# Kernel optimization log

Measured on AMD Instinct MI355X. Metric: run time of the kernel, lower is better.

Reference implementation:

```python
import jax, jax.numpy as jnp
import numpy as np

B, N, IN_DIM, OUT_DIM, MID_DIM, K = 4, 8192, 3, 64, 32, 16
EPS = 1e-5  # BatchNorm eps


def _bn_relu(x, gamma, beta):
    # x: [B, N, C]; BatchNorm1d in training mode -> batch stats over (B, N)
    mean = jnp.mean(x, axis=(0, 1))
    var = jnp.var(x, axis=(0, 1))
    return jax.nn.relu(gamma * (x - mean) * jax.lax.rsqrt(var + EPS) + beta)


def _gather(pts, idx):
    # pts: [B, N, C]; idx: [B, ...] int -> [B, ..., C]
    return jax.vmap(lambda p, i: p[i])(pts, idx)


def _fps(xyz, npoint):
    # farthest point sampling; xyz: [B, N, 3] -> idx [B, npoint]
    b, n, _ = xyz.shape

    def step(carry, _):
        dist, farthest = carry
        centroid = jnp.take_along_axis(xyz, farthest[:, None, None], axis=1)  # [B,1,3]
        d = jnp.sum((xyz - centroid) ** 2, axis=-1)  # [B,N]
        dist = jnp.minimum(dist, d)
        nxt = jnp.argmax(dist, axis=-1).astype(jnp.int32)
        return (dist, nxt), farthest

    init = (jnp.full((b, n), 1e10, xyz.dtype), jnp.zeros((b,), jnp.int32))
    _, idx = jax.lax.scan(step, init, None, length=npoint)
    return idx.T  # [B, npoint]


def _knn(query, ref, k):
    # query: [B,S,3], ref: [B,N,3] -> k nearest indices [B,S,k]
    d = (jnp.sum(query ** 2, -1, keepdims=True)
         - 2.0 * jnp.einsum('bsd,bnd->bsn', query, ref)
         + jnp.sum(ref ** 2, -1)[:, None, :])
    _, idx = jax.lax.top_k(-d, k)
    return idx


def setup_inputs() -> dict:
    key = jax.random.key(0)
    ks = jax.random.split(key, 13)
    sc = lambda fan_in: 1.0 / np.sqrt(fan_in)
    inp = {
        'x_in': jax.random.normal(ks[0], (B, N, IN_DIM), jnp.float32),
        # first_mlp: Conv1d(3,32,1) -> BN -> ReLU -> Conv1d(32,64,1)
        'W1': jax.random.uniform(ks[1], (MID_DIM, IN_DIM), jnp.float32, -sc(IN_DIM), sc(IN_DIM)),
        'b1': jax.random.uniform(ks[2], (MID_DIM,), jnp.float32, -sc(IN_DIM), sc(IN_DIM)),
        'g1': jnp.ones((MID_DIM,), jnp.float32),
        'be1': jnp.zeros((MID_DIM,), jnp.float32),
        'W2': jax.random.uniform(ks[3], (OUT_DIM, MID_DIM), jnp.float32, -sc(MID_DIM), sc(MID_DIM)),
        'b2': jax.random.uniform(ks[4], (OUT_DIM,), jnp.float32, -sc(MID_DIM), sc(MID_DIM)),
        # last_mlp: Conv1d(67,64,1) -> BN -> ReLU -> Conv1d(64,64,1)
        'W3': jax.random.uniform(ks[5], (OUT_DIM, OUT_DIM + IN_DIM), jnp.float32, -sc(OUT_DIM + IN_DIM), sc(OUT_DIM + IN_DIM)),
        'b3': jax.random.uniform(ks[6], (OUT_DIM,), jnp.float32, -sc(OUT_DIM + IN_DIM), sc(OUT_DIM + IN_DIM)),
        'g2': jnp.ones((OUT_DIM,), jnp.float32),
        'be2': jnp.zeros((OUT_DIM,), jnp.float32),
        'W4': jax.random.uniform(ks[7], (OUT_DIM, OUT_DIM), jnp.float32, -sc(OUT_DIM), sc(OUT_DIM)),
        'b4': jax.random.uniform(ks[8], (OUT_DIM,), jnp.float32, -sc(OUT_DIM), sc(OUT_DIM)),
    }
    return inp


def reference(x_in, W1, b1, g1, be1, W2, b2, W3, b3, g2, be2, W4, b4):
    # first_mlp (1x1 convs == per-point matmuls), [B,N,3] -> [B,N,64]
    h = _bn_relu(x_in @ W1.T + b1, g1, be1)
    feat = h @ W2.T + b2  # [B,N,64]

    # sample_and_group: FPS to N//2 centers, kNN grouping (indices are non-diff)
    xyz_c = jax.lax.stop_gradient(x_in)
    npoint = N // 2
    fidx = _fps(xyz_c, npoint)                      # [B,S]
    new_xyz = _gather(x_in, fidx)                   # [B,S,3]
    idx = _knn(_gather(xyz_c, fidx), xyz_c, K)      # [B,S,K]

    grouped_xyz = _gather(x_in, idx) - new_xyz[:, :, None, :]  # [B,S,K,3]
    grouped_feat = _gather(feat, idx)                          # [B,S,K,64]
    x_cat = jnp.concatenate([grouped_xyz, grouped_feat], axis=-1)  # [B,S,K,67]

    x = jnp.max(x_cat, axis=2)  # max over neighbors -> [B,S,67]

    # last_mlp, [B,S,67] -> [B,S,64]
    x = _bn_relu(x @ W3.T + b3, g2, be2)
    return x @ W4.T + b4
```

## Files before the change

### kernel.cpp

```cpp
#include <hip/hip_runtime.h>
#include <float.h>
#include <math.h>

#define NB 4
#define NPTS 8192
#define NS 4096
#define MIDC 32
#define OUTC 64
#define CATC 67
#define BN_EPS 1e-5f
#define TOTAL_PTS (NB*NPTS)
#define TOTAL_S (NB*NS)


__device__ __forceinline__ double packkey(double d, int sp) {
    return __longlong_as_double((__double_as_longlong(d) & 0xFFFFFFFFFFFFE000ULL)
                                | (unsigned long long)sp);
}

template<int CTRL, int RM>
__device__ __forceinline__ double dpp_fmax64(double v) {
    int lo = __builtin_amdgcn_update_dpp(0, __double2loint(v), CTRL, RM, 0xF, false);
    int hi = __builtin_amdgcn_update_dpp(0, __double2hiint(v), CTRL, RM, 0xF, false);
    return fmax(v, __hiloint2double(hi, lo));
}

__global__ void k_first(const float* __restrict__ xin, const float* __restrict__ W1,
                        const float* __restrict__ b1, float* __restrict__ t1) {
    int p = blockIdx.x * blockDim.x + threadIdx.x;
    float x = xin[p * 3], y = xin[p * 3 + 1], z = xin[p * 3 + 2];
#pragma unroll
    for (int c = 0; c < MIDC; c++) {
        float v = fmaf(W1[c * 3 + 2], z, fmaf(W1[c * 3 + 1], y, fmaf(W1[c * 3], x, b1[c])));
        t1[c * TOTAL_PTS + p] = v;
    }
}

__global__ void k_stats1(const float* __restrict__ t1, float* __restrict__ stats) {
    int c = blockIdx.x, tid = threadIdx.x;
    if (tid < 8) stats[64 + c * 8 + tid] = 0.f;
    float s = 0.f, ss = 0.f;
    for (int i = tid; i < TOTAL_PTS; i += 256) {
        float v = t1[c * TOTAL_PTS + i];
        s += v; ss = fmaf(v, v, ss);
    }
#pragma unroll
    for (int off = 32; off; off >>= 1) { s += __shfl_down(s, off); ss += __shfl_down(ss, off); }
    __shared__ float ls[4], lss[4];
    int w = tid >> 6, lane = tid & 63;
    if (lane == 0) { ls[w] = s; lss[w] = ss; }
    __syncthreads();
    if (tid == 0) {
        s = ls[0] + ls[1] + ls[2] + ls[3];
        ss = lss[0] + lss[1] + lss[2] + lss[3];
        float m = s / (float)TOTAL_PTS;
        float var = ss / (float)TOTAL_PTS - m * m;
        stats[c] = m;
        stats[32 + c] = rsqrtf(var + BN_EPS);
    }
}

__global__ void __launch_bounds__(256) k_feat(const float* __restrict__ t1, const float* __restrict__ stats,
                                              const float* __restrict__ g1, const float* __restrict__ be1,
                                              const float* __restrict__ W2, const float* __restrict__ b2,
                                              float* __restrict__ feat) {
    __shared__ float W2s[OUTC * MIDC];
    for (int i = threadIdx.x; i < OUTC * MIDC; i += 256) W2s[i] = W2[i];
    __syncthreads();
    int p = blockIdx.x * blockDim.x + threadIdx.x;
    float h[MIDC];
#pragma unroll
    for (int c = 0; c < MIDC; c++) {
        float v = t1[c * TOTAL_PTS + p];
        v = fmaf((v - stats[c]) * stats[32 + c], g1[c], be1[c]);
        h[c] = fmaxf(v, 0.f);
    }
#pragma unroll 4
    for (int o = 0; o < OUTC; o++) {
        float a = b2[o];
#pragma unroll
        for (int c = 0; c < MIDC; c++) a = fmaf(W2s[o * MIDC + c], h[c], a);
        feat[p * OUTC + o] = a;
    }
}

__device__ __forceinline__ unsigned int mpart(unsigned int x) {
    x &= 1023u;
    x = (x | (x << 16)) & 0x030000FFu;
    x = (x | (x << 8))  & 0x0300F00Fu;
    x = (x | (x << 4))  & 0x030C30C3u;
    x = (x | (x << 2))  & 0x09249249u;
    return x;
}

__global__ void __launch_bounds__(1024, 4) k_fps(const float* __restrict__ xin, int* __restrict__ fidx) {
    const int b = blockIdx.x;
    const int tid = threadIdx.x;
    const int lane = tid & 63, w = tid >> 6;
    const float* xb = xin + (size_t)b * NPTS * 3;
    __shared__ union UU {
        struct SS {
            float4 spts[NPTS];
            double swd[2][16];
            float  bbx[16][6];
        } s;
        unsigned long long karr[NPTS];
    } u;

    float mnx = FLT_MAX, mny = FLT_MAX, mnz = FLT_MAX;
    float mxx = -FLT_MAX, mxy = -FLT_MAX, mxz = -FLT_MAX;
    for (int j = 0; j < 8; j++) {
        int p = tid + (j << 10);
        float x = xb[p * 3], y = xb[p * 3 + 1], z = xb[p * 3 + 2];
        mnx = fminf(mnx, x); mny = fminf(mny, y); mnz = fminf(mnz, z);
        mxx = fmaxf(mxx, x); mxy = fmaxf(mxy, y); mxz = fmaxf(mxz, z);
    }
#pragma unroll
    for (int off = 32; off; off >>= 1) {
        mnx = fminf(mnx, __shfl_xor(mnx, off)); mny = fminf(mny, __shfl_xor(mny, off));
        mnz = fminf(mnz, __shfl_xor(mnz, off));
        mxx = fmaxf(mxx, __shfl_xor(mxx, off)); mxy = fmaxf(mxy, __shfl_xor(mxy, off));
        mxz = fmaxf(mxz, __shfl_xor(mxz, off));
    }
    if (lane == 0) {
        u.s.bbx[w][0] = mnx; u.s.bbx[w][1] = mny; u.s.bbx[w][2] = mnz;
        u.s.bbx[w][3] = mxx; u.s.bbx[w][4] = mxy; u.s.bbx[w][5] = mxz;
    }
    __syncthreads();
#pragma unroll
    for (int i = 0; i < 16; i++) {
        mnx = fminf(mnx, u.s.bbx[i][0]); mny = fminf(mny, u.s.bbx[i][1]);
        mnz = fminf(mnz, u.s.bbx[i][2]);
        mxx = fmaxf(mxx, u.s.bbx[i][3]); mxy = fmaxf(mxy, u.s.bbx[i][4]);
        mxz = fmaxf(mxz, u.s.bbx[i][5]);
    }
    float scx = 1023.0f / fmaxf(mxx - mnx, 1e-20f);
    float scy = 1023.0f / fmaxf(mxy - mny, 1e-20f);
    float scz = 1023.0f / fmaxf(mxz - mnz, 1e-20f);
    __syncthreads();

    for (int j = 0; j < 8; j++) {
        int p = tid + (j << 10);
        float x = xb[p * 3], y = xb[p * 3 + 1], z = xb[p * 3 + 2];
        unsigned int ix = (unsigned int)min(1023, max(0, (int)((x - mnx) * scx)));
        unsigned int iy = (unsigned int)min(1023, max(0, (int)((y - mny) * scy)));
        unsigned int iz = (unsigned int)min(1023, max(0, (int)((z - mnz) * scz)));
        unsigned long long code = (unsigned long long)((mpart(ix) << 2) | (mpart(iy) << 1) | mpart(iz));
        u.karr[p] = (code << 13) | (unsigned long long)p;
    }
    __syncthreads();
    for (int k = 2; k <= NPTS; k <<= 1) {
        for (int jj = k >> 1; jj > 0; jj >>= 1) {
            for (int pos = tid; pos < NPTS; pos += 1024) {
                int l2 = pos ^ jj;
                if (l2 > pos) {
                    unsigned long long a = u.karr[pos], c = u.karr[l2];
                    bool up = ((pos & k) == 0);
                    if ((up && a > c) || (!up && a < c)) { u.karr[pos] = c; u.karr[l2] = a; }
                }
            }
            __syncthreads();
        }
    }

    unsigned long long kk[8];
#pragma unroll
    for (int j = 0; j < 8; j++) kk[j] = u.karr[tid * 8 + j];
    __syncthreads();
    float blox = FLT_MAX, bloy = FLT_MAX, bloz = FLT_MAX;
    float bhix = -FLT_MAX, bhiy = -FLT_MAX, bhiz = -FLT_MAX;
    float prx[8], pry[8], prz[8];
    double dk[8];
#pragma unroll
    for (int j = 0; j < 8; j++) {
        int oi = (int)(kk[j] & 0x1FFFULL);
        float x = xb[oi * 3], y = xb[oi * 3 + 1], z = xb[oi * 3 + 2];
        int sp = tid * 8 + j;
        int slot = (sp >> 3) | ((sp & 7) << 10);
        u.s.spts[slot] = make_float4(x, y, z, __int_as_float(oi));
        prx[j] = x; pry[j] = y; prz[j] = z;
        blox = fminf(blox, x); bloy = fminf(bloy, y); bloz = fminf(bloz, z);
        bhix = fmaxf(bhix, x); bhiy = fmaxf(bhiy, y); bhiz = fmaxf(bhiz, z);
        dk[j] = packkey(1e10, sp);
    }
    if (tid == 0) fidx[b * NS] = 0;
    __syncthreads();

    float cxf = xb[0], cyf = xb[1], czf = xb[2];
    double cx = (double)cxf, cy = (double)cyf, cz = (double)czf;
    double tmax = packkey(1e10, tid * 8 + 7);
    double wm = 0.0;
    for (int t = 1; t < NS; t++) {
        float exf = fmaxf(fmaxf(blox - cxf, cxf - bhix), 0.f);
        float eyf = fmaxf(fmaxf(bloy - cyf, cyf - bhiy), 0.f);
        float ezf = fmaxf(fmaxf(bloz - czf, czf - bhiz), 0.f);
        float dmsqf = fmaf(exf, exf, fmaf(eyf, eyf, ezf * ezf));
        double tupper = __longlong_as_double(__double_as_longlong(tmax) | 0x1FFFULL);
        bool doupd = !((double)dmsqf * 0.99999 > tupper);
        if (__any(doupd)) {
            if (doupd) {
                double t0 = 0.0, t1 = 0.0;
#pragma unroll
                for (int j = 0; j < 8; j += 2) {
                    double dx0 = (double)prx[j] - cx, dy0 = (double)pry[j] - cy, dz0 = (double)prz[j] - cz;
                    double d0 = fma(dx0, dx0, fma(dy0, dy0, dz0 * dz0));
                    double nk0 = fmin(dk[j], packkey(d0, tid * 8 + j));
                    dk[j] = nk0; t0 = fmax(t0, nk0);
                    double dx1 = (double)prx[j + 1] - cx, dy1 = (double)pry[j + 1] - cy, dz1 = (double)prz[j + 1] - cz;
                    double d1 = fma(dx1, dx1, fma(dy1, dy1, dz1 * dz1));
                    double nk1 = fmin(dk[j + 1], packkey(d1, tid * 8 + j + 1));
                    dk[j + 1] = nk1; t1 = fmax(t1, nk1);
                }
                tmax = fmax(t0, t1);
            }
            double v = tmax;
            v = dpp_fmax64<0x121, 0xF>(v);
            v = dpp_fmax64<0x122, 0xF>(v);
            v = dpp_fmax64<0x124, 0xF>(v);
            v = dpp_fmax64<0x128, 0xF>(v);
            v = dpp_fmax64<0x142, 0xa>(v);
            v = dpp_fmax64<0x143, 0x8>(v);
            int wlo = __builtin_amdgcn_readlane(__double2loint(v), 63);
            int whi = __builtin_amdgcn_readlane(__double2hiint(v), 63);
            wm = __hiloint2double(whi, wlo);
        }
        if (lane == 0) u.s.swd[t & 1][w] = wm;
        __syncthreads();
        double gv = u.s.swd[t & 1][lane & 15];
        gv = dpp_fmax64<0x121, 0xF>(gv);
        gv = dpp_fmax64<0x122, 0xF>(gv);
        gv = dpp_fmax64<0x124, 0xF>(gv);
        gv = dpp_fmax64<0x128, 0xF>(gv);
        int sp = (int)((unsigned int)__double_as_longlong(gv) & 0x1FFFu);
        float4 cw = u.s.spts[(sp >> 3) | ((sp & 7) << 10)];
        cxf = cw.x; cyf = cw.y; czf = cw.z;
        cx = (double)cxf; cy = (double)cyf; cz = (double)czf;
        if (tid == 0) fidx[b * NS + t] = __float_as_int(cw.w);
    }
}

#define KT2 1024
__global__ void __launch_bounds__(256) k_knn(const float* __restrict__ xin, const int* __restrict__ fidx,
                                             int* __restrict__ knn) {
    __shared__ double sxd[KT2], syd[KT2], szd[KT2];
    __shared__ double mk[4][16][64];
    int tid = threadIdx.x;
    int part = tid >> 6;
    int ql = tid & 63;
    int gq = blockIdx.x * 64 + ql;
    int b = gq >> 12;
    const float* xb = xin + (size_t)b * NPTS * 3;
    int qi = fidx[gq];
    double qx = (double)xb[qi * 3], qy = (double)xb[qi * 3 + 1], qz = (double)xb[qi * 3 + 2];
    double kd0 = DBL_MAX, kd1 = DBL_MAX, kd2 = DBL_MAX, kd3 = DBL_MAX,
           kd4 = DBL_MAX, kd5 = DBL_MAX, kd6 = DBL_MAX, kd7 = DBL_MAX,
           kd8 = DBL_MAX, kd9 = DBL_MAX, kd10 = DBL_MAX, kd11 = DBL_MAX,
           kd12 = DBL_MAX, kd13 = DBL_MAX, kd14 = DBL_MAX, kd15 = DBL_MAX;
    for (int tile = 0; tile < NPTS / KT2; tile++) {
        for (int m = tid; m < KT2; m += 256) {
            int gj = tile * KT2 + m;
            sxd[m] = (double)xb[gj * 3];
            syd[m] = (double)xb[gj * 3 + 1];
            szd[m] = (double)xb[gj * 3 + 2];
        }
        __syncthreads();
        int base = part * (KT2 / 4);
        for (int m = 0; m < KT2 / 4; m++) {
            int li = base + m;
            double dx = qx - sxd[li], dy = qy - syd[li], dz = qz - szd[li];
            double d = fma(dx, dx, fma(dy, dy, dz * dz));
            double key = __longlong_as_double(
                (__double_as_longlong(d) & 0xFFFFFFFFFFFFE000ULL)
                | (unsigned long long)(tile * KT2 + li));
            if (key < kd15) {
                kd15 = fmax(kd14, fmin(kd15, key)); kd14 = fmax(kd13, fmin(kd14, key));
                kd13 = fmax(kd12, fmin(kd13, key)); kd12 = fmax(kd11, fmin(kd12, key));
                kd11 = fmax(kd10, fmin(kd11, key)); kd10 = fmax(kd9,  fmin(kd10, key));
                kd9  = fmax(kd8,  fmin(kd9,  key)); kd8  = fmax(kd7,  fmin(kd8,  key));
                kd7  = fmax(kd6,  fmin(kd7,  key)); kd6  = fmax(kd5,  fmin(kd6,  key));
                kd5  = fmax(kd4,  fmin(kd5,  key)); kd4  = fmax(kd3,  fmin(kd4,  key));
                kd3  = fmax(kd2,  fmin(kd3,  key)); kd2  = fmax(kd1,  fmin(kd2,  key));
                kd1  = fmax(kd0,  fmin(kd1,  key)); kd0  = fmin(kd0,  key);
            }
        }
        __syncthreads();
    }
    mk[part][0][ql] = kd0;  mk[part][1][ql] = kd1;  mk[part][2][ql] = kd2;  mk[part][3][ql] = kd3;
    mk[part][4][ql] = kd4;  mk[part][5][ql] = kd5;  mk[part][6][ql] = kd6;  mk[part][7][ql] = kd7;
    mk[part][8][ql] = kd8;  mk[part][9][ql] = kd9;  mk[part][10][ql] = kd10; mk[part][11][ql] = kd11;
    mk[part][12][ql] = kd12; mk[part][13][ql] = kd13; mk[part][14][ql] = kd14; mk[part][15][ql] = kd15;
    __syncthreads();
    if (tid < 64) {
        int i0 = 0, i1 = 0, i2 = 0, i3 = 0;
        double h0 = mk[0][0][tid], h1 = mk[1][0][tid], h2 = mk[2][0][tid], h3 = mk[3][0][tid];
        int* outp = knn + (size_t)(blockIdx.x * 64 + tid) * 16;
#pragma unroll
        for (int k = 0; k < 16; k++) {
            double mm = fmin(fmin(h0, h1), fmin(h2, h3));
            outp[k] = (int)(__double_as_longlong(mm) & 0x1FFFULL);
            if (mm == h0)      { i0++; h0 = (i0 < 16) ? mk[0][i0][tid] : DBL_MAX; }
            else if (mm == h1) { i1++; h1 = (i1 < 16) ? mk[1][i1][tid] : DBL_MAX; }
            else if (mm == h2) { i2++; h2 = (i2 < 16) ? mk[2][i2][tid] : DBL_MAX; }
            else               { i3++; h3 = (i3 < 16) ? mk[3][i3][tid] : DBL_MAX; }
        }
    }
}

__global__ void __launch_bounds__(256) k_group(const float* __restrict__ xin, const float* __restrict__ feat,
                                               const int* __restrict__ fidx, const int* __restrict__ knn,
                                               const float* __restrict__ W3, const float* __restrict__ b3,
                                               float* __restrict__ y3, float* __restrict__ stats) {
    __shared__ float W3s[OUTC * CATC];
    __shared__ float x67[4][68];
    __shared__ float lsum[64], lsq[64];
    int tid = threadIdx.x, w = tid >> 6, lane = tid & 63;
    for (int i = tid; i < OUTC * CATC; i += 256) W3s[i] = W3[i];
    if (tid < 64) { lsum[tid] = 0.f; lsq[tid] = 0.f; }
    __syncthreads();
    float psum = 0.f, psq = 0.f;
    int p0 = blockIdx.x * 64 + w * 16;
    for (int it = 0; it < 16; it++) {
        int p = p0 + it;
        int b = p >> 12;
        int myidx = knn[p * 16 + (lane & 15)];
        int nbk[16];
#pragma unroll
        for (int k = 0; k < 16; k++) nbk[k] = __shfl(myidx, k);
        float m = -FLT_MAX;
#pragma unroll
        for (int k = 0; k < 16; k++) m = fmaxf(m, feat[(size_t)(b * NPTS + nbk[k]) * OUTC + lane]);
        x67[w][3 + lane] = m;
        if (lane < 3) {
            int ci = fidx[p];
            float cc = xin[(size_t)(b * NPTS + ci) * 3 + lane];
            float mg = -FLT_MAX;
#pragma unroll
            for (int k = 0; k < 16; k++) mg = fmaxf(mg, xin[(size_t)(b * NPTS + nbk[k]) * 3 + lane] - cc);
            x67[w][lane] = mg;
        }
        __syncthreads();
        float acc = b3[lane];
#pragma unroll
        for (int c = 0; c < CATC; c++) acc = fmaf(W3s[lane * CATC + c], x67[w][c], acc);
        y3[(size_t)p * OUTC + lane] = acc;
        psum += acc; psq = fmaf(acc, acc, psq);
        __syncthreads();
    }
    atomicAdd(&lsum[lane], psum);
    atomicAdd(&lsq[lane], psq);
    __syncthreads();
    if (tid < 64) { atomicAdd(&stats[64 + tid], lsum[tid]); atomicAdd(&stats[128 + tid], lsq[tid]); }
}

__global__ void k_stats2(float* __restrict__ stats) {
    int c = threadIdx.x;
    float m = stats[64 + c] / (float)TOTAL_S;
    float var = stats[128 + c] / (float)TOTAL_S - m * m;
    stats[192 + c] = m;
    stats[256 + c] = rsqrtf(var + BN_EPS);
}

__global__ void __launch_bounds__(256) k_last(const float* __restrict__ y3, const float* __restrict__ stats,
                                              const float* __restrict__ g2, const float* __restrict__ be2,
                                              const float* __restrict__ W4, const float* __restrict__ b4,
                                              float* __restrict__ out) {
    __shared__ float W4t[OUTC * OUTC];
    __shared__ float xs[4][64];
    int tid = threadIdx.x;
    for (int i = tid; i < OUTC * OUTC; i += 256) W4t[(i & 63) * 64 + (i >> 6)] = W4[i];
    int lp = tid >> 6, o = tid & 63;
    int p = blockIdx.x * 4 + lp;
    float v = y3[(size_t)p * OUTC + o];
    v = fmaf((v - stats[192 + o]) * stats[256 + o], g2[o], be2[o]);
    xs[lp][o] = fmaxf(v, 0.f);
    __syncthreads();
    const float* xp = xs[lp];
    float acc = b4[o];
#pragma unroll
    for (int c = 0; c < OUTC; c++) acc = fmaf(W4t[c * 64 + o], xp[c], acc);
    out[(size_t)p * OUTC + o] = acc;
}

extern "C" void kernel_launch(void* const* d_in, const int* in_sizes, int n_in,
                              void* d_out, int out_size, void* d_ws, size_t ws_size,
                              hipStream_t stream) {
    const float* xin = (const float*)d_in[0];
    const float* W1  = (const float*)d_in[1];
    const float* b1  = (const float*)d_in[2];
    const float* g1  = (const float*)d_in[3];
    const float* be1 = (const float*)d_in[4];
    const float* W2  = (const float*)d_in[5];
    const float* b2  = (const float*)d_in[6];
    const float* W3  = (const float*)d_in[7];
    const float* b3  = (const float*)d_in[8];
    const float* g2  = (const float*)d_in[9];
    const float* be2 = (const float*)d_in[10];
    const float* W4  = (const float*)d_in[11];
    const float* b4  = (const float*)d_in[12];
    float* out = (float*)d_out;

    float* ws = (float*)d_ws;
    float* t1   = ws;
    float* feat = t1 + (size_t)MIDC * TOTAL_PTS;
    int*   fidx = (int*)(feat + (size_t)TOTAL_PTS * OUTC);
    int*   knn  = fidx + TOTAL_S;
    float* y3   = (float*)(knn + (size_t)TOTAL_S * 16);
    float* stats = y3 + (size_t)TOTAL_S * OUTC;

    k_first<<<TOTAL_PTS / 256, 256, 0, stream>>>(xin, W1, b1, t1);
    k_stats1<<<MIDC, 256, 0, stream>>>(t1, stats);
    k_feat<<<TOTAL_PTS / 256, 256, 0, stream>>>(t1, stats, g1, be1, W2, b2, feat);
    k_fps<<<NB, 1024, 0, stream>>>(xin, fidx);
    k_knn<<<TOTAL_S / 64, 256, 0, stream>>>(xin, fidx, knn);
    k_group<<<TOTAL_S / 64, 256, 0, stream>>>(xin, feat, fidx, knn, W3, b3, y3, stats);
    k_stats2<<<1, 64, 0, stream>>>(stats);
    k_last<<<TOTAL_S / 4, 256, 0, stream>>>(y3, stats, g2, be2, W4, b4, out);
}
```

Before: 3.782 ms.

## Derive BN1 stats from input moments, prefilter kNN in fp32, trim syncs

The first BatchNorm's mean and variance are now computed analytically from the 3D input's first and second moments, accumulated in double, so the 32-channel intermediate buffer, its stats pass and its reload all go away. The feature kernel recomputes the linear layer on the fly with a folded scale and shift. In kNN the tile is stored as floats, and an fp32 distance check against a slightly inflated threshold skips most double-precision key work. FPS reads point coordinates from shared memory instead of registers, lowering register pressure at the cost of LDS loads, and k_group drops two block barriers that appear unnecessary because each wave uses only its own x67 row. Risks are precision differences in the moment-based variance and any ordering dependence the removed barriers were covering.

```diff
diff --git a/kernel.cpp b/kernel.cpp
--- a/kernel.cpp
+++ b/kernel.cpp
@@ -25,55 +25,70 @@
     return fmax(v, __hiloint2double(hi, lo));
 }
 
-__global__ void k_first(const float* __restrict__ xin, const float* __restrict__ W1,
-                        const float* __restrict__ b1, float* __restrict__ t1) {
-    int p = blockIdx.x * blockDim.x + threadIdx.x;
+__global__ void k_init(float* __restrict__ stats, double* __restrict__ mom) {
+    int tid = threadIdx.x;
+    if (tid < 128) stats[64 + tid] = 0.f;
+    if (tid < 9) mom[tid] = 0.0;
+}
+
+__global__ void __launch_bounds__(256) k_mom(const float* __restrict__ xin, double* __restrict__ mom) {
+    int t = blockIdx.x * 256 + threadIdx.x;
+    double sx = 0, sy = 0, sz = 0, sxx = 0, sxy = 0, sxz = 0, syy = 0, syz = 0, szz = 0;
+#pragma unroll
+    for (int j = 0; j < 4; j++) {
+        int p = t * 4 + j;
+        double x = (double)xin[p * 3], y = (double)xin[p * 3 + 1], z = (double)xin[p * 3 + 2];
+        sx += x; sy += y; sz += z;
+        sxx = fma(x, x, sxx); sxy = fma(x, y, sxy); sxz = fma(x, z, sxz);
+        syy = fma(y, y, syy); syz = fma(y, z, syz); szz = fma(z, z, szz);
+    }
+#pragma unroll
+    for (int off = 32; off; off >>= 1) {
+        sx += __shfl_down(sx, off); sy += __shfl_down(sy, off); sz += __shfl_down(sz, off);
+        sxx += __shfl_down(sxx, off); sxy += __shfl_down(sxy, off); sxz += __shfl_down(sxz, off);
+        syy += __shfl_down(syy, off); syz += __shfl_down(syz, off); szz += __shfl_down(szz, off);
+    }
+    if ((threadIdx.x & 63) == 0) {
+        atomicAdd(&mom[0], sx); atomicAdd(&mom[1], sy); atomicAdd(&mom[2], sz);
+        atomicAdd(&mom[3], sxx); atomicAdd(&mom[4], sxy); atomicAdd(&mom[5], sxz);
+        atomicAdd(&mom[6], syy); atomicAdd(&mom[7], syz); atomicAdd(&mom[8], szz);
+    }
+}
+
+__global__ void k_bn1stats(const double* __restrict__ mom, const float* __restrict__ W1,
+                           const float* __restrict__ b1, float* __restrict__ stats) {
+    int c = threadIdx.x;
+    double n = (double)TOTAL_PTS;
+    double mx = mom[0] / n, my = mom[1] / n, mz = mom[2] / n;
+    double Cxx = mom[3] / n - mx * mx, Cxy = mom[4] / n - mx * my, Cxz = mom[5] / n - mx * mz;
+    double Cyy = mom[6] / n - my * my, Cyz = mom[7] / n - my * mz, Czz = mom[8] / n - mz * mz;
+    double wx = (double)W1[c * 3], wy = (double)W1[c * 3 + 1], wz = (double)W1[c * 3 + 2];
+    double mu = wx * mx + wy * my + wz * mz + (double)b1[c];
+    double var = wx * wx * Cxx + wy * wy * Cyy + wz * wz * Czz
+               + 2.0 * (wx * wy * Cxy + wx * wz * Cxz + wy * wz * Cyz);
+    stats[c] = (float)mu;
+    stats[32 + c] = rsqrtf(fmaxf((float)var, 0.f) + BN_EPS);
+}
+
+__global__ void __launch_bounds__(256) k_featx(const float* __restrict__ xin, const float* __restrict__ stats,
+                                               const float* __restrict__ W1, const float* __restrict__ b1,
+                                               const float* __restrict__ g1, const float* __restrict__ be1,
+                                               const float* __restrict__ W2, const float* __restrict__ b2,
+                                               float* __restrict__ feat) {
+    __shared__ float W2s[OUTC * MIDC];
+    __shared__ float w1s[MIDC * 3], p1[MIDC], p2[MIDC];
+    int tid = threadIdx.x;
+    for (int i = tid; i < OUTC * MIDC; i += 256) W2s[i] = W2[i];
+    if (tid < MIDC * 3) w1s[tid] = W1[tid];
+    if (tid < MIDC) { p1[tid] = stats[32 + tid] * g1[tid]; p2[tid] = be1[tid] - stats[tid] * stats[32 + tid] * g1[tid]; }
+    __syncthreads();
+    int p = blockIdx.x * blockDim.x + tid;
     float x = xin[p * 3], y = xin[p * 3 + 1], z = xin[p * 3 + 2];
+    float h[MIDC];
 #pragma unroll
     for (int c = 0; c < MIDC; c++) {
-        float v = fmaf(W1[c * 3 + 2], z, fmaf(W1[c * 3 + 1], y, fmaf(W1[c * 3], x, b1[c])));
-        t1[c * TOTAL_PTS + p] = v;
-    }
-}
-
-__global__ void k_stats1(const float* __restrict__ t1, float* __restrict__ stats) {
-    int c = blockIdx.x, tid = threadIdx.x;
-    if (tid < 8) stats[64 + c * 8 + tid] = 0.f;
-    float s = 0.f, ss = 0.f;
-    for (int i = tid; i < TOTAL_PTS; i += 256) {
-        float v = t1[c * TOTAL_PTS + i];
-        s += v; ss = fmaf(v, v, ss);
-    }
-#pragma unroll
-    for (int off = 32; off; off >>= 1) { s += __shfl_down(s, off); ss += __shfl_down(ss, off); }
-    __shared__ float ls[4], lss[4];
-    int w = tid >> 6, lane = tid & 63;
-    if (lane == 0) { ls[w] = s; lss[w] = ss; }
-    __syncthreads();
-    if (tid == 0) {
-        s = ls[0] + ls[1] + ls[2] + ls[3];
-        ss = lss[0] + lss[1] + lss[2] + lss[3];
-        float m = s / (float)TOTAL_PTS;
-        float var = ss / (float)TOTAL_PTS - m * m;
-        stats[c] = m;
-        stats[32 + c] = rsqrtf(var + BN_EPS);
-    }
-}
-
-__global__ void __launch_bounds__(256) k_feat(const float* __restrict__ t1, const float* __restrict__ stats,
-                                              const float* __restrict__ g1, const float* __restrict__ be1,
-                                              const float* __restrict__ W2, const float* __restrict__ b2,
-                                              float* __restrict__ feat) {
-    __shared__ float W2s[OUTC * MIDC];
-    for (int i = threadIdx.x; i < OUTC * MIDC; i += 256) W2s[i] = W2[i];
-    __syncthreads();
-    int p = blockIdx.x * blockDim.x + threadIdx.x;
-    float h[MIDC];
-#pragma unroll
-    for (int c = 0; c < MIDC; c++) {
-        float v = t1[c * TOTAL_PTS + p];
-        v = fmaf((v - stats[c]) * stats[32 + c], g1[c], be1[c]);
-        h[c] = fmaxf(v, 0.f);
+        float v = fmaf(w1s[c * 3 + 2], z, fmaf(w1s[c * 3 + 1], y, fmaf(w1s[c * 3], x, b1[c])));
+        h[c] = fmaxf(fmaf(v, p1[c], p2[c]), 0.f);
     }
 #pragma unroll 4
     for (int o = 0; o < OUTC; o++) {
@@ -169,7 +184,6 @@
     __syncthreads();
     float blox = FLT_MAX, bloy = FLT_MAX, bloz = FLT_MAX;
     float bhix = -FLT_MAX, bhiy = -FLT_MAX, bhiz = -FLT_MAX;
-    float prx[8], pry[8], prz[8];
     double dk[8];
 #pragma unroll
     for (int j = 0; j < 8; j++) {
@@ -178,7 +192,6 @@
         int sp = tid * 8 + j;
         int slot = (sp >> 3) | ((sp & 7) << 10);
         u.s.spts[slot] = make_float4(x, y, z, __int_as_float(oi));
-        prx[j] = x; pry[j] = y; prz[j] = z;
         blox = fminf(blox, x); bloy = fminf(bloy, y); bloz = fminf(bloz, z);
         bhix = fmaxf(bhix, x); bhiy = fmaxf(bhiy, y); bhiz = fmaxf(bhiz, z);
         dk[j] = packkey(1e10, sp);
@@ -202,11 +215,13 @@
                 double t0 = 0.0, t1 = 0.0;
 #pragma unroll
                 for (int j = 0; j < 8; j += 2) {
-                    double dx0 = (double)prx[j] - cx, dy0 = (double)pry[j] - cy, dz0 = (double)prz[j] - cz;
+                    float4 v0 = u.s.spts[tid | (j << 10)];
+                    float4 v1 = u.s.spts[tid | ((j + 1) << 10)];
+                    double dx0 = (double)v0.x - cx, dy0 = (double)v0.y - cy, dz0 = (double)v0.z - cz;
                     double d0 = fma(dx0, dx0, fma(dy0, dy0, dz0 * dz0));
                     double nk0 = fmin(dk[j], packkey(d0, tid * 8 + j));
                     dk[j] = nk0; t0 = fmax(t0, nk0);
-                    double dx1 = (double)prx[j + 1] - cx, dy1 = (double)pry[j + 1] - cy, dz1 = (double)prz[j + 1] - cz;
+                    double dx1 = (double)v1.x - cx, dy1 = (double)v1.y - cy, dz1 = (double)v1.z - cz;
                     double d1 = fma(dx1, dx1, fma(dy1, dy1, dz1 * dz1));
                     double nk1 = fmin(dk[j + 1], packkey(d1, tid * 8 + j + 1));
                     dk[j + 1] = nk1; t1 = fmax(t1, nk1);
@@ -242,7 +257,7 @@
 #define KT2 1024
 __global__ void __launch_bounds__(256) k_knn(const float* __restrict__ xin, const int* __restrict__ fidx,
                                              int* __restrict__ knn) {
-    __shared__ double sxd[KT2], syd[KT2], szd[KT2];
+    __shared__ float sxf[KT2], syf[KT2], szf[KT2];
     __shared__ double mk[4][16][64];
     int tid = threadIdx.x;
     int part = tid >> 6;
@@ -251,36 +266,42 @@
     int b = gq >> 12;
     const float* xb = xin + (size_t)b * NPTS * 3;
     int qi = fidx[gq];
-    double qx = (double)xb[qi * 3], qy = (double)xb[qi * 3 + 1], qz = (double)xb[qi * 3 + 2];
+    float qxf = xb[qi * 3], qyf = xb[qi * 3 + 1], qzf = xb[qi * 3 + 2];
+    double qx = (double)qxf, qy = (double)qyf, qz = (double)qzf;
     double kd0 = DBL_MAX, kd1 = DBL_MAX, kd2 = DBL_MAX, kd3 = DBL_MAX,
            kd4 = DBL_MAX, kd5 = DBL_MAX, kd6 = DBL_MAX, kd7 = DBL_MAX,
            kd8 = DBL_MAX, kd9 = DBL_MAX, kd10 = DBL_MAX, kd11 = DBL_MAX,
            kd12 = DBL_MAX, kd13 = DBL_MAX, kd14 = DBL_MAX, kd15 = DBL_MAX;
+    float kd15f = FLT_MAX;
     for (int tile = 0; tile < NPTS / KT2; tile++) {
         for (int m = tid; m < KT2; m += 256) {
             int gj = tile * KT2 + m;
-            sxd[m] = (double)xb[gj * 3];
-            syd[m] = (double)xb[gj * 3 + 1];
-            szd[m] = (double)xb[gj * 3 + 2];
+            sxf[m] = xb[gj * 3]; syf[m] = xb[gj * 3 + 1]; szf[m] = xb[gj * 3 + 2];
         }
         __syncthreads();
         int base = part * (KT2 / 4);
         for (int m = 0; m < KT2 / 4; m++) {
             int li = base + m;
-            double dx = qx - sxd[li], dy = qy - syd[li], dz = qz - szd[li];
-            double d = fma(dx, dx, fma(dy, dy, dz * dz));
-            double key = __longlong_as_double(
-                (__double_as_longlong(d) & 0xFFFFFFFFFFFFE000ULL)
-                | (unsigned long long)(tile * KT2 + li));
-            if (key < kd15) {
-                kd15 = fmax(kd14, fmin(kd15, key)); kd14 = fmax(kd13, fmin(kd14, key));
-                kd13 = fmax(kd12, fmin(kd13, key)); kd12 = fmax(kd11, fmin(kd12, key));
-                kd11 = fmax(kd10, fmin(kd11, key)); kd10 = fmax(kd9,  fmin(kd10, key));
-                kd9  = fmax(kd8,  fmin(kd9,  key)); kd8  = fmax(kd7,  fmin(kd8,  key));
-                kd7  = fmax(kd6,  fmin(kd7,  key)); kd6  = fmax(kd5,  fmin(kd6,  key));
-                kd5  = fmax(kd4,  fmin(kd5,  key)); kd4  = fmax(kd3,  fmin(kd4,  key));
-                kd3  = fmax(kd2,  fmin(kd3,  key)); kd2  = fmax(kd1,  fmin(kd2,  key));
-                kd1  = fmax(kd0,  fmin(kd1,  key)); kd0  = fmin(kd0,  key);
+            float fdx = qxf - sxf[li], fdy = qyf - syf[li], fdz = qzf - szf[li];
+            float d32 = fmaf(fdx, fdx, fmaf(fdy, fdy, fdz * fdz));
+            if (d32 <= kd15f) {
+                double dx = qx - (double)sxf[li], dy = qy - (double)syf[li], dz = qz - (double)szf[li];
+                double d = fma(dx, dx, fma(dy, dy, dz * dz));
+                double key = __longlong_as_double(
+                    (__double_as_longlong(d) & 0xFFFFFFFFFFFFE000ULL)
+                    | (unsigned long long)(tile * KT2 + li));
+                if (key < kd15) {
+                    kd15 = fmax(kd14, fmin(kd15, key)); kd14 = fmax(kd13, fmin(kd14, key));
+                    kd13 = fmax(kd12, fmin(kd13, key)); kd12 = fmax(kd11, fmin(kd12, key));
+                    kd11 = fmax(kd10, fmin(kd11, key)); kd10 = fmax(kd9,  fmin(kd10, key));
+                    kd9  = fmax(kd8,  fmin(kd9,  key)); kd8  = fmax(kd7,  fmin(kd8,  key));
+                    kd7  = fmax(kd6,  fmin(kd7,  key)); kd6  = fmax(kd5,  fmin(kd6,  key));
+                    kd5  = fmax(kd4,  fmin(kd5,  key)); kd4  = fmax(kd3,  fmin(kd4,  key));
+                    kd3  = fmax(kd2,  fmin(kd3,  key)); kd2  = fmax(kd1,  fmin(kd2,  key));
+                    kd1  = fmax(kd0,  fmin(kd1,  key)); kd0  = fmin(kd0,  key);
+                    kd15f = (kd15 >= DBL_MAX) ? FLT_MAX
+                          : __double2float_ru(kd15) * (1.0f + 1e-5f);
+                }
             }
         }
         __syncthreads();
@@ -338,13 +359,11 @@
             for (int k = 0; k < 16; k++) mg = fmaxf(mg, xin[(size_t)(b * NPTS + nbk[k]) * 3 + lane] - cc);
             x67[w][lane] = mg;
         }
-        __syncthreads();
         float acc = b3[lane];
 #pragma unroll
         for (int c = 0; c < CATC; c++) acc = fmaf(W3s[lane * CATC + c], x67[w][c], acc);
         y3[(size_t)p * OUTC + lane] = acc;
         psum += acc; psq = fmaf(acc, acc, psq);
-        __syncthreads();
     }
     atomicAdd(&lsum[lane], psum);
     atomicAdd(&lsq[lane], psq);
@@ -400,16 +419,17 @@
     float* out = (float*)d_out;
 
     float* ws = (float*)d_ws;
-    float* t1   = ws;
-    float* feat = t1 + (size_t)MIDC * TOTAL_PTS;
+    float* feat = ws;
     int*   fidx = (int*)(feat + (size_t)TOTAL_PTS * OUTC);
     int*   knn  = fidx + TOTAL_S;
     float* y3   = (float*)(knn + (size_t)TOTAL_S * 16);
     float* stats = y3 + (size_t)TOTAL_S * OUTC;
-
-    k_first<<<TOTAL_PTS / 256, 256, 0, stream>>>(xin, W1, b1, t1);
-    k_stats1<<<MIDC, 256, 0, stream>>>(t1, stats);
-    k_feat<<<TOTAL_PTS / 256, 256, 0, stream>>>(t1, stats, g1, be1, W2, b2, feat);
+    double* mom = (double*)(stats + 320);
+
+    k_init<<<1, 256, 0, stream>>>(stats, mom);
+    k_mom<<<32, 256, 0, stream>>>(xin, mom);
+    k_bn1stats<<<1, 32, 0, stream>>>(mom, W1, b1, stats);
+    k_featx<<<TOTAL_PTS / 256, 256, 0, stream>>>(xin, stats, W1, b1, g1, be1, W2, b2, feat);
     k_fps<<<NB, 1024, 0, stream>>>(xin, fidx);
     k_knn<<<TOTAL_S / 64, 256, 0, stream>>>(xin, fidx, knn);
     k_group<<<TOTAL_S / 64, 256, 0, stream>>>(xin, feat, fidx, knn, W3, b3, y3, stats);
```

Result: slower. 4.410 ms (+16.6%).
